# Optimization experiments

Hardware: AMD Instinct MI355X
Metric: run time of the kernel (lower is better)

## Reference

```python
import jax, jax.numpy as jnp
import numpy as np


def setup_inputs() -> dict:
    key = jax.random.key(0)
    ks = jax.random.split(key, 5)
    B, S, D, H, DK = 2, 2048, 1024, 16, 64
    scale = 1.0 / np.sqrt(D)
    return {
        "x": jax.random.normal(ks[0], (B, S, D), dtype=jnp.float32),
        "Wq": jax.random.normal(ks[1], (H, D, DK), dtype=jnp.float32) * scale,
        "Wk": jax.random.normal(ks[2], (H, D, DK), dtype=jnp.float32) * scale,
        "Wv": jax.random.normal(ks[3], (H, D, DK), dtype=jnp.float32) * scale,
        "Wo": jax.random.normal(ks[4], (D, D), dtype=jnp.float32) * scale,
    }


def reference(x, Wq, Wk, Wv, Wo):
    # x: (B, S, D); Wq/Wk/Wv: (H, D, d_k); Wo: (D, D) torch-Linear convention (y = c @ Wo.T)
    B, S, D = x.shape
    H, _, dk = Wq.shape
    Q = jnp.einsum('bsd,hdk->bhsk', x, Wq)  # (B,H,S,dk)
    K = jnp.einsum('bsd,hdk->bhsk', x, Wk)
    V = jnp.einsum('bsd,hdk->bhsk', x, Wv)
    scores = jnp.einsum('bhqk,bhsk->bhqs', Q, K) / jnp.sqrt(jnp.float32(dk))  # (B,H,S,S)
    causal = jnp.tril(jnp.ones((S, S), dtype=bool))
    scores = jnp.where(causal[None, None, :, :], scores, -jnp.inf)
    weights = jax.nn.softmax(scores, axis=-1)
    out = jnp.einsum('bhqs,bhsk->bhqk', weights, V)  # (B,H,S,dk)
    concat = out.transpose(0, 2, 1, 3).reshape(B, S, H * dk)  # heads concatenated h-major
    return concat @ Wo.T
```

## Files before the change

kernel.cpp:

```cpp
#include <hip/hip_runtime.h>

typedef unsigned short u16;
typedef unsigned int u32;
typedef __bf16 bf16x8 __attribute__((ext_vector_type(8)));
typedef float f32x4 __attribute__((ext_vector_type(4)));
typedef u16 u16x8 __attribute__((ext_vector_type(8)));
typedef u16 u16x4 __attribute__((ext_vector_type(4)));
typedef u32 u32x4 __attribute__((ext_vector_type(4)));

#define NH 16
#define DKK 64
#define SQ 2048
#define DD 1024

#define AS1 __attribute__((address_space(1)))
#define AS3 __attribute__((address_space(3)))

#define QSCALE 0.1803368925f

__device__ inline u16 f2bf(float f) {
  union { float f; u32 u; } v; v.f = f;
  u32 u = v.u;
  u += 0x7FFFu + ((u >> 16) & 1u);
  return (u16)(u >> 16);
}

__device__ __forceinline__ u32 cvtpk(float lo, float hi) {
  u32 r;
  asm("v_cvt_pk_bf16_f32 %0, %1, %2" : "=v"(r) : "v"(lo), "v"(hi));
  return r;
}

__device__ inline u16x8 cvt8(const float* p) {
  float4 a = *(const float4*)p;
  float4 b = *(const float4*)(p + 4);
  u16x8 v;
  v[0] = f2bf(a.x); v[1] = f2bf(a.y); v[2] = f2bf(a.z); v[3] = f2bf(a.w);
  v[4] = f2bf(b.x); v[5] = f2bf(b.y); v[6] = f2bf(b.z); v[7] = f2bf(b.w);
  return v;
}

__device__ __forceinline__ void gload16(const u16* g, u16* l) {
  __builtin_amdgcn_global_load_lds((const AS1 u32*)(const void*)g,
                                   (AS3 u32*)(void*)l, 16, 0, 0);
}

__global__ __launch_bounds__(256) void prep_kernel(const float* __restrict__ x,
                                                   u16* __restrict__ xb,
                                                   const float* __restrict__ Wo,
                                                   u16* __restrict__ Wob,
                                                   const float* __restrict__ Wq,
                                                   const float* __restrict__ Wk,
                                                   const float* __restrict__ Wv,
                                                   u16* __restrict__ WT) {
  __shared__ u16 sm[64][72];
  int bid = blockIdx.x;
  int tid = threadIdx.x;
  if (bid < 2560) {
    const float* src; u16* dst; size_t base;
    if (bid < 2048) { src = x;  dst = xb;  base = (size_t)bid * 2048; }
    else            { src = Wo; dst = Wob; base = (size_t)(bid - 2048) * 2048; }
    size_t off = base + (size_t)tid * 8;
    *(u16x8*)&dst[off] = cvt8(&src[off]);
    return;
  }
  int wid = bid - 2560;
  int t = wid >> 8;
  int rem = wid & 255;
  int h = rem >> 4;
  int d0 = (rem & 15) * 64;
  const float* src = (t == 0) ? Wq : (t == 1) ? Wk : Wv;
  for (int j = 0; j < 2; ++j) {
    int idx = tid + j * 256;
    int r = idx >> 3;
    int c0 = (idx & 7) * 8;
    *(u16x8*)&sm[r][c0] = cvt8(&src[(h * DD + d0 + r) * DKK + c0]);
  }
  __syncthreads();
  for (int j = 0; j < 2; ++j) {
    int idx = tid + j * 256;
    int r2 = idx >> 3;
    int c0 = (idx & 7) * 8;
    u16x8 vv;
    for (int i = 0; i < 8; ++i) vv[i] = sm[c0 + i][r2];
    int n = t * 1024 + h * 64 + r2;
    *(u16x8*)&WT[n * DD + d0 + c0] = vv;
  }
}

__global__ __launch_bounds__(256) void gemm128(const u16* __restrict__ A,
                                               const u16* __restrict__ Bm,
                                               int mode,
                                               u16* __restrict__ o0,
                                               u16* __restrict__ o1,
                                               u16* __restrict__ o2,
                                               float* __restrict__ of) {
  __shared__ u16 As[128 * 32];
  __shared__ u16 Bs[128 * 32];
  const int K = 1024;
  int m0 = blockIdx.x * 128;
  int n0 = blockIdx.y * 128;
  int tid = threadIdx.x;
  int w = tid >> 6, l = tid & 63;
  int lg = l >> 4, lr = l & 15;
  int wr = w >> 1, wc = w & 1;

  int srow = w * 32 + (l >> 2);
  int sg = (l & 3) ^ ((l >> 3) & 3);
  const u16* gA = A + (size_t)(m0 + srow) * K + sg * 8;
  const u16* gB = Bm + (size_t)(n0 + srow) * K + sg * 8;
  u16* lA = As + w * 1024;
  u16* lB = Bs + w * 1024;
  int gsw = (lr >> 1) & 3;

  f32x4 acc[4][4] = {};
  for (int kt = 0; kt < 32; ++kt) {
    int k0 = kt * 32;
    gload16(gA + k0, lA);
    gload16(gA + k0 + 16 * K, lA + 512);
    gload16(gB + k0, lB);
    gload16(gB + k0 + 16 * K, lB + 512);
    __syncthreads();
    bf16x8 a[4], b[4];
    #pragma unroll
    for (int m = 0; m < 4; ++m)
      a[m] = *(const bf16x8*)&As[(wr * 64 + m * 16 + lr) * 32 + ((lg ^ gsw) * 8)];
    #pragma unroll
    for (int n = 0; n < 4; ++n)
      b[n] = *(const bf16x8*)&Bs[(wc * 64 + n * 16 + lr) * 32 + ((lg ^ gsw) * 8)];
    #pragma unroll
    for (int m = 0; m < 4; ++m)
      #pragma unroll
      for (int n = 0; n < 4; ++n)
        acc[m][n] = __builtin_amdgcn_mfma_f32_16x16x32_bf16(a[m], b[n], acc[m][n], 0, 0, 0);
    __syncthreads();
  }

  if (mode == 1) {
    int mbase = m0 + wr * 64 + lg * 4;
    int nbase = n0 + wc * 64 + lr;
    #pragma unroll
    for (int m = 0; m < 4; ++m)
      #pragma unroll
      for (int n = 0; n < 4; ++n)
        #pragma unroll
        for (int rr = 0; rr < 4; ++rr)
          of[(size_t)(mbase + m * 16 + rr) * 1024 + nbase + n * 16] = acc[m][n][rr];
  } else {
    int t = n0 >> 10;
    int h = (((n0 & 1023) + wc * 64) >> 6);
    int bq = m0 >> 11;
    int sbase = (m0 & 2047) + wr * 64 + lg * 4;
    if (t < 2) {
      float sc = (t == 0) ? QSCALE : 1.0f;
      u16* o = (t == 0) ? o0 : o1;
      u16* op = o + (size_t)(bq * NH + h) * SQ * DKK;
      #pragma unroll
      for (int m = 0; m < 4; ++m)
        #pragma unroll
        for (int n = 0; n < 4; ++n)
          #pragma unroll
          for (int rr = 0; rr < 4; ++rr)
            op[(size_t)(sbase + m * 16 + rr) * DKK + n * 16 + lr] = f2bf(acc[m][n][rr] * sc);
    } else {
      u16* op = o2 + (size_t)(bq * NH + h) * DKK * SQ;
      int Sb = (m0 & 2047) + wr * 64;
      #pragma unroll
      for (int m = 0; m < 4; ++m)
        #pragma unroll
        for (int n = 0; n < 4; ++n) {
          u16x4 vv;
          #pragma unroll
          for (int rr = 0; rr < 4; ++rr) vv[rr] = f2bf(acc[m][n][rr]);
          *(u16x4*)&op[(size_t)(n * 16 + lr) * SQ + Sb + (m >> 1) * 32 + lg * 8 + (m & 1) * 4] = vv;
        }
    }
  }
}

__global__ __launch_bounds__(256) void attn_kernel(const u16* __restrict__ Q,
                                                   const u16* __restrict__ Kg,
                                                   const u16* __restrict__ Vt,
                                                   u16* __restrict__ Cc) {
  __shared__ u16 Ks[2][64 * 64];
  __shared__ u16 Vs[2][64 * 64];
  int bh = blockIdx.x;
  int y = blockIdx.y;
  int a = y & 7, bsel = y >> 3;
  int s = (bsel == 0) ? 2 * a : (bsel == 1) ? 2 * a + 1
        : (bsel == 2) ? 30 - 2 * a : 31 - 2 * a;
  int tid = threadIdx.x;
  int w = tid >> 6, l = tid & 63;
  int lg = l >> 4, lr = l & 15;
  const u16* Qp = Q + (size_t)bh * SQ * DKK;
  const u16* Kp = Kg + (size_t)bh * SQ * DKK;
  const u16* Vp = Vt + (size_t)bh * DKK * SQ;
  int b = bh >> 4, h = bh & 15;
  int cur = 0;

  int lrow8 = l >> 3;
  int swz = (l & 7) ^ lrow8;
  int r7 = lr & 7;
  const u16* kSrc0 = Kp + (size_t)(w * 16 + lrow8) * DKK + swz * 8;
  const u16* kSrc1 = Kp + (size_t)(w * 16 + 8 + lrow8) * DKK + swz * 8;
  const u16* vSrc0 = Vp + (size_t)(w * 16 + lrow8) * SQ + swz * 8;
  const u16* vSrc1 = Vp + (size_t)(w * 16 + 8 + lrow8) * SQ + swz * 8;

  #define STAGE(buf, j0)                                                  \
    do {                                                                  \
      gload16(kSrc0 + (size_t)(j0) * DKK, &Ks[buf][(w * 16) * 64]);       \
      gload16(kSrc1 + (size_t)(j0) * DKK, &Ks[buf][(w * 16 + 8) * 64]);   \
      gload16(vSrc0 + (j0), &Vs[buf][(w * 16) * 64]);                     \
      gload16(vSrc1 + (j0), &Vs[buf][(w * 16 + 8) * 64]);                 \
    } while (0)

  STAGE(0, 0);
  __syncthreads();

  int qrow = s * 64 + w * 16 + lr;
  bf16x8 qf0 = *(const bf16x8*)&Qp[(size_t)qrow * DKK + lg * 8];
  bf16x8 qf1 = *(const bf16x8*)&Qp[(size_t)qrow * DKK + 32 + lg * 8];
  f32x4 o[4] = {};
  float mrun = -1e30f, lrun = 0.f;

  for (int jt = 0; jt <= s; ++jt) {
    if (jt < s) STAGE(cur ^ 1, (jt + 1) * 64);

    float p[16];
    __builtin_amdgcn_s_setprio(1);
    #pragma unroll
    for (int c = 0; c < 4; ++c) {
      int R = c * 16 + lr;
      const u16* kr = &Ks[cur][R * 64];
      bf16x8 k0 = *(const bf16x8*)&kr[(lg ^ r7) * 8];
      bf16x8 k1 = *(const bf16x8*)&kr[((4 + lg) ^ r7) * 8];
      f32x4 z = {};
      z = __builtin_amdgcn_mfma_f32_16x16x32_bf16(k0, qf0, z, 0, 0, 0);
      z = __builtin_amdgcn_mfma_f32_16x16x32_bf16(k1, qf1, z, 0, 0, 0);
      #pragma unroll
      for (int rr = 0; rr < 4; ++rr) p[c * 4 + rr] = z[rr];
    }
    __builtin_amdgcn_s_setprio(0);
    if (jt == s) {
      int j0 = jt * 64;
      #pragma unroll
      for (int c = 0; c < 4; ++c)
        #pragma unroll
        for (int rr = 0; rr < 4; ++rr) {
          int kv = j0 + c * 16 + lg * 4 + rr;
          if (kv > qrow) p[c * 4 + rr] = -1e30f;
        }
    }
    float t0 = fmaxf(fmaxf(p[0], p[1]), p[2]);
    float t1 = fmaxf(fmaxf(p[3], p[4]), p[5]);
    float t2 = fmaxf(fmaxf(p[6], p[7]), p[8]);
    float t3 = fmaxf(fmaxf(p[9], p[10]), p[11]);
    float t4 = fmaxf(fmaxf(p[12], p[13]), p[14]);
    float pm = fmaxf(fmaxf(fmaxf(t0, t1), fmaxf(t2, t3)), fmaxf(t4, p[15]));
    pm = fmaxf(pm, __shfl_xor(pm, 16, 64));
    pm = fmaxf(pm, __shfl_xor(pm, 32, 64));
    float alpha = 1.0f;
    if (__any(pm > mrun + 11.0f)) {
      float mnew = fmaxf(mrun, pm);
      alpha = exp2f(mrun - mnew);
      mrun = mnew;
      float af[4];
      #pragma unroll
      for (int rr = 0; rr < 4; ++rr) af[rr] = __shfl(alpha, ((l >> 4) << 2) + rr, 64);
      #pragma unroll
      for (int n = 0; n < 4; ++n)
        #pragma unroll
        for (int rr = 0; rr < 4; ++rr) o[n][rr] *= af[rr];
    }
    float su = 0.f;
    #pragma unroll
    for (int i = 0; i < 16; ++i) { p[i] = exp2f(p[i] - mrun); su += p[i]; }
    su += __shfl_xor(su, 16, 64);
    su += __shfl_xor(su, 32, 64);
    lrun = lrun * alpha + su;
    union { u32x4 w; bf16x8 v; } pk0, pk1;
    pk0.w[0] = cvtpk(p[0],  p[1]);
    pk0.w[1] = cvtpk(p[2],  p[3]);
    pk0.w[2] = cvtpk(p[4],  p[5]);
    pk0.w[3] = cvtpk(p[6],  p[7]);
    pk1.w[0] = cvtpk(p[8],  p[9]);
    pk1.w[1] = cvtpk(p[10], p[11]);
    pk1.w[2] = cvtpk(p[12], p[13]);
    pk1.w[3] = cvtpk(p[14], p[15]);
    {
      bf16x8 pa0 = pk0.v, pa1 = pk1.v;
      __builtin_amdgcn_s_setprio(1);
      #pragma unroll
      for (int n = 0; n < 4; ++n) {
        int R2 = n * 16 + lr;
        bf16x8 vb0 = *(const bf16x8*)&Vs[cur][R2 * 64 + ((lg ^ r7) * 8)];
        o[n] = __builtin_amdgcn_mfma_f32_16x16x32_bf16(pa0, vb0, o[n], 0, 0, 0);
        bf16x8 vb1 = *(const bf16x8*)&Vs[cur][R2 * 64 + (((4 + lg) ^ r7) * 8)];
        o[n] = __builtin_amdgcn_mfma_f32_16x16x32_bf16(pa1, vb1, o[n], 0, 0, 0);
      }
      __builtin_amdgcn_s_setprio(0);
    }
    __syncthreads();
    cur ^= 1;
  }

  float lrow[4];
  #pragma unroll
  for (int rr = 0; rr < 4; ++rr) lrow[rr] = __shfl(lrun, ((l >> 4) << 2) + rr, 64);
  int srow = s * 64 + w * 16 + lg * 4;
  #pragma unroll
  for (int n = 0; n < 4; ++n)
    #pragma unroll
    for (int rr = 0; rr < 4; ++rr) {
      float val = o[n][rr] / lrow[rr];
      Cc[((size_t)(b * SQ + srow + rr)) * DD + h * DKK + n * 16 + lr] = f2bf(val);
    }
  #undef STAGE
}

extern "C" void kernel_launch(void* const* d_in, const int* in_sizes, int n_in,
                              void* d_out, int out_size, void* d_ws, size_t ws_size,
                              hipStream_t stream) {
  (void)in_sizes; (void)n_in; (void)out_size; (void)ws_size;
  const float* x  = (const float*)d_in[0];
  const float* Wq = (const float*)d_in[1];
  const float* Wk = (const float*)d_in[2];
  const float* Wv = (const float*)d_in[3];
  const float* Wo = (const float*)d_in[4];
  float* out = (float*)d_out;
  u16* ws = (u16*)d_ws;
  u16* WT  = ws;
  u16* Qb  = WT + 3145728;
  u16* Kb  = Qb + 4194304;
  u16* Vb  = Kb + 4194304;
  u16* XC  = Vb + 4194304;
  u16* Wob = XC + 4194304;

  hipLaunchKernelGGL(prep_kernel, dim3(3328), dim3(256), 0, stream, x, XC, Wo, Wob, Wq, Wk, Wv, WT);
  hipLaunchKernelGGL(gemm128, dim3(32, 24), dim3(256), 0, stream, XC, WT, 0, Qb, Kb, Vb, (float*)nullptr);
  hipLaunchKernelGGL(attn_kernel, dim3(32, 32), dim3(256), 0, stream, Qb, Kb, Vb, XC);
  hipLaunchKernelGGL(gemm128, dim3(32, 8), dim3(256), 0, stream, XC, Wob, 1, nullptr, nullptr, nullptr, out);
}
```

Measured before the change: 132.7 us.

## Double GEMM K-tile to 64 and defer softmax row-sum reduction

The projection GEMM now stages a K-slice of 64 per iteration instead of 32, with an 8-way XOR swizzle on LDS. This halves the number of barrier pairs and load phases per output tile, at the cost of twice the shared memory per block, which may lower occupancy. The attention kernel keeps a per-lane partial row sum, rescaled only when the max changes, and does the cross-lane shuffle reduction once after the loop instead of every tile.

```diff
diff --git a/kernel.cpp b/kernel.cpp
--- a/kernel.cpp
+++ b/kernel.cpp
@@ -95,8 +95,8 @@
                                                u16* __restrict__ o1,
                                                u16* __restrict__ o2,
                                                float* __restrict__ of) {
-  __shared__ u16 As[128 * 32];
-  __shared__ u16 Bs[128 * 32];
+  __shared__ u16 As[128 * 64];
+  __shared__ u16 Bs[128 * 64];
   const int K = 1024;
   int m0 = blockIdx.x * 128;
   int n0 = blockIdx.y * 128;
@@ -105,34 +105,38 @@
   int lg = l >> 4, lr = l & 15;
   int wr = w >> 1, wc = w & 1;
 
-  int srow = w * 32 + (l >> 2);
-  int sg = (l & 3) ^ ((l >> 3) & 3);
+  int srow = w * 32 + (l >> 3);
+  int sg = (l & 7) ^ ((l >> 3) & 7);
   const u16* gA = A + (size_t)(m0 + srow) * K + sg * 8;
   const u16* gB = Bm + (size_t)(n0 + srow) * K + sg * 8;
-  u16* lA = As + w * 1024;
-  u16* lB = Bs + w * 1024;
-  int gsw = (lr >> 1) & 3;
+  u16* lA = As + (w * 32) * 64;
+  u16* lB = Bs + (w * 32) * 64;
+  int key = lr & 7;
 
   f32x4 acc[4][4] = {};
-  for (int kt = 0; kt < 32; ++kt) {
-    int k0 = kt * 32;
-    gload16(gA + k0, lA);
-    gload16(gA + k0 + 16 * K, lA + 512);
-    gload16(gB + k0, lB);
-    gload16(gB + k0 + 16 * K, lB + 512);
+  for (int kt = 0; kt < 16; ++kt) {
+    int k0 = kt * 64;
+    #pragma unroll
+    for (int g = 0; g < 4; ++g) {
+      gload16(gA + k0 + g * 8 * K, lA + g * 8 * 64);
+      gload16(gB + k0 + g * 8 * K, lB + g * 8 * 64);
+    }
     __syncthreads();
-    bf16x8 a[4], b[4];
-    #pragma unroll
-    for (int m = 0; m < 4; ++m)
-      a[m] = *(const bf16x8*)&As[(wr * 64 + m * 16 + lr) * 32 + ((lg ^ gsw) * 8)];
-    #pragma unroll
-    for (int n = 0; n < 4; ++n)
-      b[n] = *(const bf16x8*)&Bs[(wc * 64 + n * 16 + lr) * 32 + ((lg ^ gsw) * 8)];
-    #pragma unroll
-    for (int m = 0; m < 4; ++m)
+    #pragma unroll
+    for (int kk = 0; kk < 2; ++kk) {
+      bf16x8 a[4], b[4];
+      #pragma unroll
+      for (int m = 0; m < 4; ++m)
+        a[m] = *(const bf16x8*)&As[(wr * 64 + m * 16 + lr) * 64 + (((kk * 4 + lg) ^ key) * 8)];
       #pragma unroll
       for (int n = 0; n < 4; ++n)
-        acc[m][n] = __builtin_amdgcn_mfma_f32_16x16x32_bf16(a[m], b[n], acc[m][n], 0, 0, 0);
+        b[n] = *(const bf16x8*)&Bs[(wc * 64 + n * 16 + lr) * 64 + (((kk * 4 + lg) ^ key) * 8)];
+      #pragma unroll
+      for (int m = 0; m < 4; ++m)
+        #pragma unroll
+        for (int n = 0; n < 4; ++n)
+          acc[m][n] = __builtin_amdgcn_mfma_f32_16x16x32_bf16(a[m], b[n], acc[m][n], 0, 0, 0);
+    }
     __syncthreads();
   }
 
@@ -221,7 +225,7 @@
   bf16x8 qf0 = *(const bf16x8*)&Qp[(size_t)qrow * DKK + lg * 8];
   bf16x8 qf1 = *(const bf16x8*)&Qp[(size_t)qrow * DKK + 32 + lg * 8];
   f32x4 o[4] = {};
-  float mrun = -1e30f, lrun = 0.f;
+  float mrun = -1e30f, lpart = 0.f;
 
   for (int jt = 0; jt <= s; ++jt) {
     if (jt < s) STAGE(cur ^ 1, (jt + 1) * 64);
@@ -259,14 +263,14 @@
     float pm = fmaxf(fmaxf(fmaxf(t0, t1), fmaxf(t2, t3)), fmaxf(t4, p[15]));
     pm = fmaxf(pm, __shfl_xor(pm, 16, 64));
     pm = fmaxf(pm, __shfl_xor(pm, 32, 64));
-    float alpha = 1.0f;
     if (__any(pm > mrun + 11.0f)) {
       float mnew = fmaxf(mrun, pm);
-      alpha = exp2f(mrun - mnew);
+      float alpha = exp2f(mrun - mnew);
       mrun = mnew;
+      lpart *= alpha;
       float af[4];
       #pragma unroll
-      for (int rr = 0; rr < 4; ++rr) af[rr] = __shfl(alpha, ((l >> 4) << 2) + rr, 64);
+      for (int rr = 0; rr < 4; ++rr) af[rr] = __shfl(alpha, lg * 4 + rr, 64);
       #pragma unroll
       for (int n = 0; n < 4; ++n)
         #pragma unroll
@@ -275,9 +279,7 @@
     float su = 0.f;
     #pragma unroll
     for (int i = 0; i < 16; ++i) { p[i] = exp2f(p[i] - mrun); su += p[i]; }
-    su += __shfl_xor(su, 16, 64);
-    su += __shfl_xor(su, 32, 64);
-    lrun = lrun * alpha + su;
+    lpart += su;
     union { u32x4 w; bf16x8 v; } pk0, pk1;
     pk0.w[0] = cvtpk(p[0],  p[1]);
     pk0.w[1] = cvtpk(p[2],  p[3]);
@@ -304,9 +306,12 @@
     cur ^= 1;
   }
 
+  float lsum = lpart;
+  lsum += __shfl_xor(lsum, 16, 64);
+  lsum += __shfl_xor(lsum, 32, 64);
   float lrow[4];
   #pragma unroll
-  for (int rr = 0; rr < 4; ++rr) lrow[rr] = __shfl(lrun, ((l >> 4) << 2) + rr, 64);
+  for (int rr = 0; rr < 4; ++rr) lrow[rr] = __shfl(lsum, lg * 4 + rr, 64);
   int srow = s * 64 + w * 16 + lg * 4;
   #pragma unroll
   for (int n = 0; n < 4; ++n)
```

Result: faster. 123.1 us (-7.2%).
